# Kernel tuning notes

Hardware: AMD Instinct MI355X
Metric: run time of the kernel (lower is better)

The kernel has to match this reference:

```python
import jax, jax.numpy as jnp
import numpy as np

B, T, H, L = 64, 512, 768, 30


def _make_ent_ids(rng, b, t):
    # two contiguous entity spans per example, like the tokenizer-produced mask
    ent = np.zeros((b, t), dtype=np.int32)
    for i in range(b):
        s1 = int(rng.integers(1, t // 2 - 20)); l1 = int(rng.integers(2, 12))
        s2 = int(rng.integers(t // 2, t - 20)); l2 = int(rng.integers(2, 12))
        ent[i, s1:s1 + l1] = 1
        ent[i, s2:s2 + l2] = 1
    return ent


def setup_inputs() -> dict:
    key = jax.random.key(0)
    ks = jax.random.split(key, 8)
    rng = np.random.default_rng(0)
    sc = 0.02
    return {
        "last_hidden_states": jax.random.normal(ks[0], (B, T, H), jnp.float32),
        "pooled_output": jax.random.normal(ks[1], (B, H), jnp.float32),
        "ent_ids": jnp.asarray(_make_ent_ids(rng, B, T)),
        "labels": jax.random.randint(ks[2], (B,), 0, L, dtype=jnp.int32),
        "W_cls": jax.random.normal(ks[3], (H, H), jnp.float32) * sc,
        "b_cls": jnp.zeros((H,), jnp.float32),
        "W_e1": jax.random.normal(ks[4], (H, H), jnp.float32) * sc,
        "b_e1": jnp.zeros((H,), jnp.float32),
        "W_e2": jax.random.normal(ks[5], (H, H), jnp.float32) * sc,
        "b_e2": jnp.zeros((H,), jnp.float32),
        "W_cat": jax.random.normal(ks[6], (3 * H, L), jnp.float32) * sc,
        "b_cat": jnp.zeros((L,), jnp.float32),
    }


def _span_means(h, ent_ids):
    # Vectorized replacement for the per-batch Python loop: label each
    # contiguous run of 1s in ent_ids with its run index (1 = entity1,
    # 2 = entity2), then mean-pool hidden states over each run.
    prev = jnp.pad(ent_ids, ((0, 0), (1, 0)))[:, :-1]        # [B,T] shifted right
    starts = ((ent_ids == 1) & (prev == 0)).astype(jnp.int32)
    span_id = jnp.cumsum(starts, axis=1) * ent_ids           # 0 / 1 / 2
    m1 = (span_id == 1).astype(h.dtype)                      # [B,T]
    m2 = (span_id == 2).astype(h.dtype)
    c1 = jnp.maximum(jnp.sum(m1, axis=1, keepdims=True), 1.0)
    c2 = jnp.maximum(jnp.sum(m2, axis=1, keepdims=True), 1.0)
    e1 = jnp.einsum('bt,bth->bh', m1, h) / c1                # mean over span 1
    e2 = jnp.einsum('bt,bth->bh', m2, h) / c2                # mean over span 2 (0 if absent)
    return e1, e2


def reference(last_hidden_states, pooled_output, ent_ids, labels,
              W_cls, b_cls, W_e1, b_e1, W_e2, b_e2, W_cat, b_cat):
    e1, e2 = _span_means(last_hidden_states, ent_ids)
    p = pooled_output @ W_cls + b_cls
    o1 = jnp.tanh(e1) @ W_e1 + b_e1
    o2 = jnp.tanh(e2) @ W_e2 + b_e2
    logits = jnp.concatenate([p, o1, o2], axis=1) @ W_cat + b_cat
    probs = jax.nn.softmax(logits, axis=1)          # module applies Softmax to logits
    # CrossEntropyLoss is then applied on top of the softmax output (as in source)
    logp = jax.nn.log_softmax(probs, axis=1)
    loss = -jnp.mean(jnp.take_along_axis(logp, labels[:, None].astype(jnp.int32), axis=1))
    return probs, loss
```

## Files before the change

kernel.cpp:

```cpp
#include <hip/hip_runtime.h>
#include <hip/hip_bf16.h>
#include <math.h>

#define NB 64
#define NTOK 512
#define NH 768
#define NL 30
#define NLP 32
#define AST 776
#define MAXSPAN 12
#define MAGIC 0x5F3A9C71u

typedef __attribute__((ext_vector_type(8))) short short8;
typedef __attribute__((ext_vector_type(4))) float f32x4;
typedef __attribute__((ext_vector_type(4))) unsigned int u32x4;

__device__ inline unsigned short f2bf(float f) {
    union { float f; unsigned int u; } v; v.f = f;
    unsigned int u = v.u;
    return (unsigned short)((u + 0x7fffu + ((u >> 16) & 1u)) >> 16);
}
__device__ inline unsigned int pack2(float a, float b) {
    return (unsigned int)f2bf(a) | ((unsigned int)f2bf(b) << 16);
}
__device__ inline float bflo(unsigned int v) {
    union { unsigned int u; float f; } c; c.u = v << 16; return c.f;
}
__device__ inline float bfhi(unsigned int v) {
    union { unsigned int u; float f; } c; c.u = v & 0xffff0000u; return c.f;
}

struct PhA { unsigned short Al[NLP * AST]; f32x4 Red[8 * 64]; };
struct PhS { int ents[NTOK]; float xsh[3 * NH]; float lgsh[NLP];
             int s1, s2, c1, c2; };
struct PhR { float red[NLP]; };
union Sh1 { PhA a; PhS s; PhR r; };

__global__ __launch_bounds__(256)
void kfused(const float* __restrict__ hs, const float* __restrict__ pooled,
            const int* __restrict__ ent, const int* __restrict__ labels,
            const float* __restrict__ Wcls, const float* __restrict__ bcls,
            const float* __restrict__ We1,  const float* __restrict__ be1,
            const float* __restrict__ We2,  const float* __restrict__ be2,
            const float* __restrict__ Wcat, const float* __restrict__ bcat,
            unsigned short* __restrict__ Wcbb, float* __restrict__ bcW,
            float* __restrict__ lws, unsigned int* __restrict__ flags,
            float* __restrict__ out)
{
    __shared__ Sh1 sh;
    const int bx = blockIdx.x, tid = threadIdx.x;

    if (bx < 144) {
        const int m = bx / 48, ht = bx % 48, h0 = ht * 16;
        const float* Wm = (m == 0) ? Wcls : (m == 1) ? We1 : We2;
        const float* Wc = Wcat + (size_t)m * NH * NL;
        #pragma unroll
        for (int i = 0; i < 48; ++i) {
            int p = tid + i * 256;
            int l = p & 31, kp = p >> 5;
            float g0 = 0.f, g1 = 0.f;
            if (l < NL) {
                g0 = Wc[(size_t)(2 * kp)     * NL + l];
                g1 = Wc[(size_t)(2 * kp + 1) * NL + l];
            }
            *(unsigned int*)&sh.a.Al[l * AST + 2 * kp] = pack2(g0, g1);
        }
        __syncthreads();
        const int w = tid >> 6, lane = tid & 63;
        const int l15 = lane & 15, kg = lane >> 4;
        const int kb0 = w * 192;
        f32x4 acc0 = {0.f,0.f,0.f,0.f}, acc1 = {0.f,0.f,0.f,0.f};
        const float* wrow = Wm + (size_t)(h0 + l15) * NH + kb0 + kg * 8;
        #pragma unroll
        for (int s = 0; s < 6; ++s) {
            f32x4 b0 = *(const f32x4*)(wrow + s * 32);
            f32x4 b1 = *(const f32x4*)(wrow + s * 32 + 4);
            union { short8 s8; unsigned int u[4]; } bb;
            bb.u[0] = pack2(b0[0], b0[1]); bb.u[1] = pack2(b0[2], b0[3]);
            bb.u[2] = pack2(b1[0], b1[1]); bb.u[3] = pack2(b1[2], b1[3]);
            const int ka = kb0 + s * 32 + kg * 8;
            short8 a0 = *(const short8*)&sh.a.Al[l15 * AST + ka];
            short8 a1 = *(const short8*)&sh.a.Al[(16 + l15) * AST + ka];
            acc0 = __builtin_amdgcn_mfma_f32_16x16x32_bf16(a0, bb.s8, acc0, 0, 0, 0);
            acc1 = __builtin_amdgcn_mfma_f32_16x16x32_bf16(a1, bb.s8, acc1, 0, 0, 0);
        }
        __syncthreads();
        sh.a.Red[(w * 2 + 0) * 64 + lane] = acc0;
        sh.a.Red[(w * 2 + 1) * 64 + lane] = acc1;
        __syncthreads();
        {
            const int l = tid >> 3, hp = tid & 7;
            const int lrow = l & 15, a = l >> 4;
            const int ln0 = (lrow >> 2) * 16 + 2 * hp;
            const int j = lrow & 3;
            float v0 = 0.f, v1 = 0.f;
            #pragma unroll
            for (int w2 = 0; w2 < 4; ++w2) {
                v0 += sh.a.Red[(w2 * 2 + a) * 64 + ln0][j];
                v1 += sh.a.Red[(w2 * 2 + a) * 64 + ln0 + 1][j];
            }
            __hip_atomic_store(
                (unsigned int*)&Wcbb[(size_t)(m * NLP + l) * NH + h0 + 2 * hp],
                pack2(v0, v1), __ATOMIC_RELAXED, __HIP_MEMORY_SCOPE_AGENT);
        }
        __syncthreads();
        if (tid == 0)
            __hip_atomic_store(&flags[bx], MAGIC, __ATOMIC_RELAXED,
                               __HIP_MEMORY_SCOPE_AGENT);
    } else if (bx < 147) {
        const int m = bx - 144;
        const float* bv = (m == 0) ? bcls : (m == 1) ? be1 : be2;
        const float* Wc = Wcat + (size_t)m * NH * NL;
        float acc[NL];
        #pragma unroll
        for (int l = 0; l < NL; ++l) acc[l] = 0.f;
        for (int k = tid; k < NH; k += 256) {
            const float v = bv[k];
            const float* wr = Wc + (size_t)k * NL;
            #pragma unroll
            for (int l = 0; l < NL; ++l) acc[l] += v * wr[l];
        }
        if (tid < NLP) sh.r.red[tid] = 0.f;
        __syncthreads();
        #pragma unroll
        for (int l = 0; l < NL; ++l) {
            float v = acc[l];
            v += __shfl_xor(v, 32); v += __shfl_xor(v, 16); v += __shfl_xor(v, 8);
            v += __shfl_xor(v, 4);  v += __shfl_xor(v, 2);  v += __shfl_xor(v, 1);
            acc[l] = v;
        }
        if ((tid & 63) == 0) {
            #pragma unroll
            for (int l = 0; l < NL; ++l) atomicAdd(&sh.r.red[l], acc[l]);
        }
        __syncthreads();
        if (tid < NL)
            __hip_atomic_store(&bcW[m * NLP + tid], sh.r.red[tid],
                               __ATOMIC_RELAXED, __HIP_MEMORY_SCOPE_AGENT);
        __syncthreads();
        if (tid == 0)
            __hip_atomic_store(&flags[bx], MAGIC, __ATOMIC_RELAXED,
                               __HIP_MEMORY_SCOPE_AGENT);
    } else if (bx < 211) {
        const int b = bx - 147;
        ((int2*)sh.s.ents)[tid] = ((const int2*)(ent + (size_t)b * NTOK))[tid];
        if (tid == 0) { sh.s.s1 = 1 << 30; sh.s.s2 = 1 << 30; sh.s.c1 = 0; sh.s.c2 = 0; }
        __syncthreads();
        bool st[2]; int tt[2];
        #pragma unroll
        for (int u = 0; u < 2; ++u) {
            int t = 2 * tid + u; tt[u] = t;
            st[u] = (sh.s.ents[t] != 0) && (t == 0 || sh.s.ents[t - 1] == 0);
            if (st[u]) atomicMin(&sh.s.s1, t);
        }
        __syncthreads();
        #pragma unroll
        for (int u = 0; u < 2; ++u)
            if (st[u] && tt[u] != sh.s.s1) atomicMin(&sh.s.s2, tt[u]);
        __syncthreads();
        #pragma unroll
        for (int u = 0; u < 2; ++u)
            if (st[u]) {
                int t = tt[u], c = 0;
                while (t + c < NTOK && sh.s.ents[t + c]) ++c;
                if (t == sh.s.s1) sh.s.c1 = c;
                else if (t == sh.s.s2) sh.s.c2 = c;
            }
        __syncthreads();
        int s1 = sh.s.s1, c1 = sh.s.c1, s2 = sh.s.s2, c2 = sh.s.c2;
        if (s1 >= NTOK) s1 = 0;
        if (s2 >= NTOK) s2 = 0;
        const float i1 = 1.0f / (float)(c1 > 0 ? c1 : 1);
        const float i2 = 1.0f / (float)(c2 > 0 ? c2 : 1);
        const int cm1 = (c1 > 0) ? c1 - 1 : 0, cm2 = (c2 > 0) ? c2 - 1 : 0;
        #pragma unroll
        for (int u = 0; u < 3; ++u) {
            const int hd = tid + u * 256;
            float a1 = 0.f, a2 = 0.f;
            #pragma unroll
            for (int j = 0; j < MAXSPAN; ++j) {
                int r1 = s1 + ((j <= cm1) ? j : cm1);
                int r2 = s2 + ((j <= cm2) ? j : cm2);
                float v1 = hs[((size_t)b * NTOK + r1) * NH + hd];
                float v2 = hs[((size_t)b * NTOK + r2) * NH + hd];
                a1 += (j < c1) ? v1 : 0.f;
                a2 += (j < c2) ? v2 : 0.f;
            }
            sh.s.xsh[0 * NH + hd] = pooled[b * NH + hd];
            sh.s.xsh[1 * NH + hd] = tanhf(a1 * i1);
            sh.s.xsh[2 * NH + hd] = tanhf(a2 * i2);
        }
        __syncthreads();
        if (tid < 147) {
            while (__hip_atomic_load(&flags[tid], __ATOMIC_RELAXED,
                                     __HIP_MEMORY_SCOPE_AGENT) != MAGIC)
                __builtin_amdgcn_s_sleep(2);
        }
        __syncthreads();
        __builtin_amdgcn_fence(__ATOMIC_ACQUIRE, "agent");
        {
            const int l = tid >> 3, ks = (tid & 7) * 96;
            float p = 0.f;
            #pragma unroll
            for (int m = 0; m < 3; ++m) {
                const unsigned short* wr = Wcbb + (size_t)(m * NLP + l) * NH + ks;
                const float* xr = &sh.s.xsh[m * NH + ks];
                #pragma unroll
                for (int i = 0; i < 12; ++i) {
                    u32x4 wv = *(const u32x4*)(wr + i * 8);
                    #pragma unroll
                    for (int q = 0; q < 4; ++q)
                        p += bflo(wv[q]) * xr[i * 8 + q * 2]
                           + bfhi(wv[q]) * xr[i * 8 + q * 2 + 1];
                }
            }
            p += __shfl_xor(p, 4); p += __shfl_xor(p, 2); p += __shfl_xor(p, 1);
            if ((tid & 7) == 0) sh.s.lgsh[l] = p;
        }
        __syncthreads();
        if (tid < 64) {
            const int l = tid;
            float lg = (l < NL)
                     ? sh.s.lgsh[l] + bcW[l] + bcW[NLP + l] + bcW[2 * NLP + l] + bcat[l]
                     : -1e30f;
            float mx = lg;
            #pragma unroll
            for (int d = 32; d >= 1; d >>= 1) mx = fmaxf(mx, __shfl_xor(mx, d));
            float e = (l < NL) ? __expf(lg - mx) : 0.f;
            float ssum = e;
            #pragma unroll
            for (int d = 32; d >= 1; d >>= 1) ssum += __shfl_xor(ssum, d);
            const float pr = e / ssum;
            if (l < NL) out[b * NL + l] = pr;
            float p2 = (l < NL) ? pr : -1e30f;
            float mx2 = p2;
            #pragma unroll
            for (int d = 32; d >= 1; d >>= 1) mx2 = fmaxf(mx2, __shfl_xor(mx2, d));
            float e2 = (l < NL) ? __expf(p2 - mx2) : 0.f;
            float s2 = e2;
            #pragma unroll
            for (int d = 32; d >= 1; d >>= 1) s2 += __shfl_xor(s2, d);
            if (l == labels[b])
                __hip_atomic_store(&lws[b],
                                   -(p2 - (mx2 + __logf(s2))) * (1.0f / (float)NB),
                                   __ATOMIC_RELAXED, __HIP_MEMORY_SCOPE_AGENT);
        }
        __syncthreads();
        if (tid == 0)
            __hip_atomic_store(&flags[160 + b], MAGIC, __ATOMIC_RELAXED,
                               __HIP_MEMORY_SCOPE_AGENT);
    } else {
        if (tid < 64) {
            while (__hip_atomic_load(&flags[160 + tid], __ATOMIC_RELAXED,
                                     __HIP_MEMORY_SCOPE_AGENT) != MAGIC)
                __builtin_amdgcn_s_sleep(2);
            float v = __hip_atomic_load(&lws[tid], __ATOMIC_RELAXED,
                                        __HIP_MEMORY_SCOPE_AGENT);
            v += __shfl_xor(v, 32); v += __shfl_xor(v, 16); v += __shfl_xor(v, 8);
            v += __shfl_xor(v, 4);  v += __shfl_xor(v, 2);  v += __shfl_xor(v, 1);
            if (tid == 0) out[NB * NL] = v;
        }
    }
}

extern "C" void kernel_launch(void* const* d_in, const int* in_sizes, int n_in,
                              void* d_out, int out_size, void* d_ws, size_t ws_size,
                              hipStream_t stream)
{
    const float* hs     = (const float*)d_in[0];
    const float* pooled = (const float*)d_in[1];
    const int*   ent    = (const int*)d_in[2];
    const int*   labels = (const int*)d_in[3];
    const float* Wcls   = (const float*)d_in[4];
    const float* bcls   = (const float*)d_in[5];
    const float* We1    = (const float*)d_in[6];
    const float* be1    = (const float*)d_in[7];
    const float* We2    = (const float*)d_in[8];
    const float* be2    = (const float*)d_in[9];
    const float* Wcat   = (const float*)d_in[10];
    const float* bcat   = (const float*)d_in[11];
    float* outp = (float*)d_out;

    unsigned short* Wcbb = (unsigned short*)d_ws;
    float* bcW = (float*)((char*)d_ws + 147456);
    float* lws = (float*)((char*)d_ws + 147456 + 384);
    unsigned int* flags = (unsigned int*)((char*)d_ws + 147456 + 384 + 256);

    kfused<<<212, 256, 0, stream>>>(hs, pooled, ent, labels, Wcls, bcls,
                                    We1, be1, We2, be2, Wcat, bcat,
                                    Wcbb, bcW, lws, flags, outp);
}
```

Baseline: 16.76 us.

## Double block size to 512 threads and repartition work across all block roles

Raises the fused kernel's block size from 256 to 512 threads and re-splits every phase: the weight-fold MFMA blocks use 8 waves with half the K range each plus an 8-way LDS reduction, the per-batch blocks handle one token per thread and use 16-way logit partials. Shared memory for the A tile and the reduction buffer is now overlaid in a union so the larger reduction fits. The flag poll is issued early so its latency overlaps span detection. The aim is more memory-level parallelism per block on a latency-bound grid, at the cost of more waves per CU, a deeper reduction and idle threads in some phases.

```diff
diff --git a/kernel.cpp b/kernel.cpp
--- a/kernel.cpp
+++ b/kernel.cpp
@@ -10,6 +10,7 @@
 #define AST 776
 #define MAXSPAN 12
 #define MAGIC 0x5F3A9C71u
+#define NT 512
 
 typedef __attribute__((ext_vector_type(8))) short short8;
 typedef __attribute__((ext_vector_type(4))) float f32x4;
@@ -30,13 +31,18 @@
     union { unsigned int u; float f; } c; c.u = v & 0xffff0000u; return c.f;
 }
 
-struct PhA { unsigned short Al[NLP * AST]; f32x4 Red[8 * 64]; };
+struct PhA {
+    union {
+        unsigned short Al[NLP * AST];
+        f32x4 Red[16 * 64];
+    } u;
+};
 struct PhS { int ents[NTOK]; float xsh[3 * NH]; float lgsh[NLP];
              int s1, s2, c1, c2; };
 struct PhR { float red[NLP]; };
 union Sh1 { PhA a; PhS s; PhR r; };
 
-__global__ __launch_bounds__(256)
+__global__ __launch_bounds__(NT)
 void kfused(const float* __restrict__ hs, const float* __restrict__ pooled,
             const int* __restrict__ ent, const int* __restrict__ labels,
             const float* __restrict__ Wcls, const float* __restrict__ bcls,
@@ -55,49 +61,49 @@
         const float* Wm = (m == 0) ? Wcls : (m == 1) ? We1 : We2;
         const float* Wc = Wcat + (size_t)m * NH * NL;
         #pragma unroll
-        for (int i = 0; i < 48; ++i) {
-            int p = tid + i * 256;
+        for (int i = 0; i < 24; ++i) {
+            int p = tid + i * NT;
             int l = p & 31, kp = p >> 5;
             float g0 = 0.f, g1 = 0.f;
             if (l < NL) {
                 g0 = Wc[(size_t)(2 * kp)     * NL + l];
                 g1 = Wc[(size_t)(2 * kp + 1) * NL + l];
             }
-            *(unsigned int*)&sh.a.Al[l * AST + 2 * kp] = pack2(g0, g1);
+            *(unsigned int*)&sh.a.u.Al[l * AST + 2 * kp] = pack2(g0, g1);
         }
         __syncthreads();
         const int w = tid >> 6, lane = tid & 63;
         const int l15 = lane & 15, kg = lane >> 4;
-        const int kb0 = w * 192;
+        const int kb0 = w * 96;
         f32x4 acc0 = {0.f,0.f,0.f,0.f}, acc1 = {0.f,0.f,0.f,0.f};
         const float* wrow = Wm + (size_t)(h0 + l15) * NH + kb0 + kg * 8;
         #pragma unroll
-        for (int s = 0; s < 6; ++s) {
+        for (int s = 0; s < 3; ++s) {
             f32x4 b0 = *(const f32x4*)(wrow + s * 32);
             f32x4 b1 = *(const f32x4*)(wrow + s * 32 + 4);
             union { short8 s8; unsigned int u[4]; } bb;
             bb.u[0] = pack2(b0[0], b0[1]); bb.u[1] = pack2(b0[2], b0[3]);
             bb.u[2] = pack2(b1[0], b1[1]); bb.u[3] = pack2(b1[2], b1[3]);
             const int ka = kb0 + s * 32 + kg * 8;
-            short8 a0 = *(const short8*)&sh.a.Al[l15 * AST + ka];
-            short8 a1 = *(const short8*)&sh.a.Al[(16 + l15) * AST + ka];
+            short8 a0 = *(const short8*)&sh.a.u.Al[l15 * AST + ka];
+            short8 a1 = *(const short8*)&sh.a.u.Al[(16 + l15) * AST + ka];
             acc0 = __builtin_amdgcn_mfma_f32_16x16x32_bf16(a0, bb.s8, acc0, 0, 0, 0);
             acc1 = __builtin_amdgcn_mfma_f32_16x16x32_bf16(a1, bb.s8, acc1, 0, 0, 0);
         }
         __syncthreads();
-        sh.a.Red[(w * 2 + 0) * 64 + lane] = acc0;
-        sh.a.Red[(w * 2 + 1) * 64 + lane] = acc1;
-        __syncthreads();
-        {
+        sh.a.u.Red[(w * 2 + 0) * 64 + lane] = acc0;
+        sh.a.u.Red[(w * 2 + 1) * 64 + lane] = acc1;
+        __syncthreads();
+        if (tid < 256) {
             const int l = tid >> 3, hp = tid & 7;
             const int lrow = l & 15, a = l >> 4;
             const int ln0 = (lrow >> 2) * 16 + 2 * hp;
             const int j = lrow & 3;
             float v0 = 0.f, v1 = 0.f;
             #pragma unroll
-            for (int w2 = 0; w2 < 4; ++w2) {
-                v0 += sh.a.Red[(w2 * 2 + a) * 64 + ln0][j];
-                v1 += sh.a.Red[(w2 * 2 + a) * 64 + ln0 + 1][j];
+            for (int w2 = 0; w2 < 8; ++w2) {
+                v0 += sh.a.u.Red[(w2 * 2 + a) * 64 + ln0][j];
+                v1 += sh.a.u.Red[(w2 * 2 + a) * 64 + ln0 + 1][j];
             }
             __hip_atomic_store(
                 (unsigned int*)&Wcbb[(size_t)(m * NLP + l) * NH + h0 + 2 * hp],
@@ -114,7 +120,7 @@
         float acc[NL];
         #pragma unroll
         for (int l = 0; l < NL; ++l) acc[l] = 0.f;
-        for (int k = tid; k < NH; k += 256) {
+        for (int k = tid; k < NH; k += NT) {
             const float v = bv[k];
             const float* wr = Wc + (size_t)k * NL;
             #pragma unroll
@@ -143,29 +149,24 @@
                                __HIP_MEMORY_SCOPE_AGENT);
     } else if (bx < 211) {
         const int b = bx - 147;
-        ((int2*)sh.s.ents)[tid] = ((const int2*)(ent + (size_t)b * NTOK))[tid];
+        sh.s.ents[tid] = ent[(size_t)b * NTOK + tid];
+        unsigned int f0 = (tid < 147)
+            ? __hip_atomic_load(&flags[tid], __ATOMIC_RELAXED,
+                                __HIP_MEMORY_SCOPE_AGENT) : MAGIC;
         if (tid == 0) { sh.s.s1 = 1 << 30; sh.s.s2 = 1 << 30; sh.s.c1 = 0; sh.s.c2 = 0; }
         __syncthreads();
-        bool st[2]; int tt[2];
-        #pragma unroll
-        for (int u = 0; u < 2; ++u) {
-            int t = 2 * tid + u; tt[u] = t;
-            st[u] = (sh.s.ents[t] != 0) && (t == 0 || sh.s.ents[t - 1] == 0);
-            if (st[u]) atomicMin(&sh.s.s1, t);
-        }
-        __syncthreads();
-        #pragma unroll
-        for (int u = 0; u < 2; ++u)
-            if (st[u] && tt[u] != sh.s.s1) atomicMin(&sh.s.s2, tt[u]);
-        __syncthreads();
-        #pragma unroll
-        for (int u = 0; u < 2; ++u)
-            if (st[u]) {
-                int t = tt[u], c = 0;
-                while (t + c < NTOK && sh.s.ents[t + c]) ++c;
-                if (t == sh.s.s1) sh.s.c1 = c;
-                else if (t == sh.s.s2) sh.s.c2 = c;
-            }
+        const int e = sh.s.ents[tid];
+        const bool st = (e != 0) && (tid == 0 || sh.s.ents[tid - 1] == 0);
+        if (st) atomicMin(&sh.s.s1, tid);
+        __syncthreads();
+        if (st && tid != sh.s.s1) atomicMin(&sh.s.s2, tid);
+        __syncthreads();
+        if (st) {
+            int c = 0;
+            while (tid + c < NTOK && sh.s.ents[tid + c]) ++c;
+            if (tid == sh.s.s1) sh.s.c1 = c;
+            else if (tid == sh.s.s2) sh.s.c2 = c;
+        }
         __syncthreads();
         int s1 = sh.s.s1, c1 = sh.s.c1, s2 = sh.s.s2, c2 = sh.s.c2;
         if (s1 >= NTOK) s1 = 0;
@@ -174,39 +175,43 @@
         const float i2 = 1.0f / (float)(c2 > 0 ? c2 : 1);
         const int cm1 = (c1 > 0) ? c1 - 1 : 0, cm2 = (c2 > 0) ? c2 - 1 : 0;
         #pragma unroll
-        for (int u = 0; u < 3; ++u) {
-            const int hd = tid + u * 256;
-            float a1 = 0.f, a2 = 0.f;
-            #pragma unroll
-            for (int j = 0; j < MAXSPAN; ++j) {
-                int r1 = s1 + ((j <= cm1) ? j : cm1);
-                int r2 = s2 + ((j <= cm2) ? j : cm2);
-                float v1 = hs[((size_t)b * NTOK + r1) * NH + hd];
-                float v2 = hs[((size_t)b * NTOK + r2) * NH + hd];
-                a1 += (j < c1) ? v1 : 0.f;
-                a2 += (j < c2) ? v2 : 0.f;
-            }
-            sh.s.xsh[0 * NH + hd] = pooled[b * NH + hd];
-            sh.s.xsh[1 * NH + hd] = tanhf(a1 * i1);
-            sh.s.xsh[2 * NH + hd] = tanhf(a2 * i2);
+        for (int u = 0; u < 2; ++u) {
+            const int hd = tid + u * NT;
+            if (hd < NH) {
+                float a1 = 0.f, a2 = 0.f;
+                #pragma unroll
+                for (int j = 0; j < MAXSPAN; ++j) {
+                    int r1 = s1 + ((j <= cm1) ? j : cm1);
+                    int r2 = s2 + ((j <= cm2) ? j : cm2);
+                    float v1 = hs[((size_t)b * NTOK + r1) * NH + hd];
+                    float v2 = hs[((size_t)b * NTOK + r2) * NH + hd];
+                    a1 += (j < c1) ? v1 : 0.f;
+                    a2 += (j < c2) ? v2 : 0.f;
+                }
+                sh.s.xsh[0 * NH + hd] = pooled[b * NH + hd];
+                sh.s.xsh[1 * NH + hd] = tanhf(a1 * i1);
+                sh.s.xsh[2 * NH + hd] = tanhf(a2 * i2);
+            }
         }
         __syncthreads();
         if (tid < 147) {
-            while (__hip_atomic_load(&flags[tid], __ATOMIC_RELAXED,
-                                     __HIP_MEMORY_SCOPE_AGENT) != MAGIC)
+            while (f0 != MAGIC) {
                 __builtin_amdgcn_s_sleep(2);
+                f0 = __hip_atomic_load(&flags[tid], __ATOMIC_RELAXED,
+                                       __HIP_MEMORY_SCOPE_AGENT);
+            }
         }
         __syncthreads();
         __builtin_amdgcn_fence(__ATOMIC_ACQUIRE, "agent");
         {
-            const int l = tid >> 3, ks = (tid & 7) * 96;
+            const int l = tid >> 4, ks = (tid & 15) * 48;
             float p = 0.f;
             #pragma unroll
             for (int m = 0; m < 3; ++m) {
                 const unsigned short* wr = Wcbb + (size_t)(m * NLP + l) * NH + ks;
                 const float* xr = &sh.s.xsh[m * NH + ks];
                 #pragma unroll
-                for (int i = 0; i < 12; ++i) {
+                for (int i = 0; i < 6; ++i) {
                     u32x4 wv = *(const u32x4*)(wr + i * 8);
                     #pragma unroll
                     for (int q = 0; q < 4; ++q)
@@ -214,8 +219,9 @@
                            + bfhi(wv[q]) * xr[i * 8 + q * 2 + 1];
                 }
             }
-            p += __shfl_xor(p, 4); p += __shfl_xor(p, 2); p += __shfl_xor(p, 1);
-            if ((tid & 7) == 0) sh.s.lgsh[l] = p;
+            p += __shfl_xor(p, 8); p += __shfl_xor(p, 4);
+            p += __shfl_xor(p, 2); p += __shfl_xor(p, 1);
+            if ((tid & 15) == 0) sh.s.lgsh[l] = p;
         }
         __syncthreads();
         if (tid < 64) {
@@ -226,18 +232,18 @@
             float mx = lg;
             #pragma unroll
             for (int d = 32; d >= 1; d >>= 1) mx = fmaxf(mx, __shfl_xor(mx, d));
-            float e = (l < NL) ? __expf(lg - mx) : 0.f;
-            float ssum = e;
+            float e2 = (l < NL) ? __expf(lg - mx) : 0.f;
+            float ssum = e2;
             #pragma unroll
             for (int d = 32; d >= 1; d >>= 1) ssum += __shfl_xor(ssum, d);
-            const float pr = e / ssum;
+            const float pr = e2 / ssum;
             if (l < NL) out[b * NL + l] = pr;
             float p2 = (l < NL) ? pr : -1e30f;
             float mx2 = p2;
             #pragma unroll
             for (int d = 32; d >= 1; d >>= 1) mx2 = fmaxf(mx2, __shfl_xor(mx2, d));
-            float e2 = (l < NL) ? __expf(p2 - mx2) : 0.f;
-            float s2 = e2;
+            float e3 = (l < NL) ? __expf(p2 - mx2) : 0.f;
+            float s2 = e3;
             #pragma unroll
             for (int d = 32; d >= 1; d >>= 1) s2 += __shfl_xor(s2, d);
             if (l == labels[b])
@@ -286,7 +292,7 @@
     float* lws = (float*)((char*)d_ws + 147456 + 384);
     unsigned int* flags = (unsigned int*)((char*)d_ws + 147456 + 384 + 256);
 
-    kfused<<<212, 256, 0, stream>>>(hs, pooled, ent, labels, Wcls, bcls,
-                                    We1, be1, We2, be2, Wcat, bcat,
-                                    Wcbb, bcW, lws, flags, outp);
-}
+    kfused<<<212, NT, 0, stream>>>(hs, pooled, ent, labels, Wcls, bcls,
+                                   We1, be1, We2, be2, Wcat, bcat,
+                                   Wcbb, bcW, lws, flags, outp);
+}
```

After: 18.76 us. +11.9%, slower.
